# Optimization experiments

Measured on AMD Instinct MI355X. Metric: run time of the kernel, lower is better.

## Reference

```python
import jax, jax.numpy as jnp
import numpy as np

N = 100000
E = 1600000
IN_DIM, HID, OUT = 128, 64, 32
SLOPE = 0.1


def setup_inputs() -> dict:
    key = jax.random.key(0)
    ks = jax.random.split(key, 8)
    x = jax.random.normal(ks[0], (N, IN_DIM), dtype=jnp.float32)
    edge_index = jax.random.randint(ks[1], (2, E), 0, N, dtype=jnp.int64)
    s1 = 1.0 / np.sqrt(IN_DIM)
    s2 = 1.0 / np.sqrt(HID)
    W_l1 = jax.random.uniform(ks[2], (IN_DIM, HID), jnp.float32, -s1, s1)
    W_r1 = jax.random.uniform(ks[3], (IN_DIM, HID), jnp.float32, -s1, s1)
    b1 = jax.random.uniform(ks[4], (HID,), jnp.float32, -s1, s1)
    W_l2 = jax.random.uniform(ks[5], (HID, OUT), jnp.float32, -s2, s2)
    W_r2 = jax.random.uniform(ks[6], (HID, OUT), jnp.float32, -s2, s2)
    b2 = jax.random.uniform(ks[7], (OUT,), jnp.float32, -s2, s2)
    return {"x": x, "edge_index": edge_index,
            "W_l1": W_l1, "W_r1": W_r1, "b1": b1,
            "W_l2": W_l2, "W_r2": W_r2, "b2": b2}


def _sage_conv(h, src, dst, deg_inv, W_l, W_r, b):
    # mean-aggregate neighbor features: gather from src, scatter-add to dst
    agg = jax.ops.segment_sum(h[src], dst, num_segments=N) * deg_inv  # [N, d]
    return agg @ W_l + h @ W_r + b


def reference(x, edge_index, W_l1, W_r1, b1, W_l2, W_r2, b2):
    src, dst = edge_index[0], edge_index[1]
    deg = jax.ops.segment_sum(jnp.ones((E,), x.dtype), dst, num_segments=N)
    deg_inv = (1.0 / jnp.maximum(deg, 1.0))[:, None]  # [N, 1]
    h = jax.nn.leaky_relu(_sage_conv(x, src, dst, deg_inv, W_l1, W_r1, b1), SLOPE)
    z = jax.nn.leaky_relu(_sage_conv(h, src, dst, deg_inv, W_l2, W_r2, b2), SLOPE)
    return z
```

## Files before the change

### kernel.cpp

```cpp
#include <hip/hip_runtime.h>


constexpr int IN_DIM  = 128;
constexpr int HID     = 64;
constexpr int OUT_DIM = 32;
constexpr float SLOPE = 0.1f;
constexpr int NPB_SHIFT = 8;
constexpr int NBMAX = 512;
constexpr int CHUNK = 4096;
constexpr int SUBCAP = 4096;

typedef unsigned int uint32;
typedef unsigned short ushort16;

__device__ inline float blo(uint32 u) { return __uint_as_float(u << 16); }
__device__ inline float bhi(uint32 u) { return __uint_as_float(u & 0xffff0000u); }
__device__ inline ushort16 f2b(float f) {
    uint32 u = __float_as_uint(f);
    u += 0x7fffu + ((u >> 16) & 1u);
    return (ushort16)(u >> 16);
}
__device__ inline uint32 pack2(float lo, float hi) {
    return (uint32)f2b(lo) | ((uint32)f2b(hi) << 16);
}
__device__ inline float lrelu(float v) { return (v > 0.f) ? v : SLOPE * v; }
__device__ inline void addup(float* acc, uint4 u) {
    acc[0] += blo(u.x); acc[1] += bhi(u.x);
    acc[2] += blo(u.y); acc[3] += bhi(u.y);
    acc[4] += blo(u.z); acc[5] += bhi(u.z);
    acc[6] += blo(u.w); acc[7] += bhi(u.w);
}

__global__ __launch_bounds__(256) void prep_kernel(
    const float* __restrict__ Wl1, const float* __restrict__ Wr1,
    const float* __restrict__ Wl2, const float* __restrict__ Wr2,
    ushort16* __restrict__ Wb1, ushort16* __restrict__ Wb2,
    int* __restrict__ bhist, int* __restrict__ done) {
    const int gid = blockIdx.x * 256 + threadIdx.x;
    if (gid < NBMAX) bhist[gid] = 0;
    if (gid == NBMAX) *done = 0;
    for (int i = gid; i < 128 * 128; i += gridDim.x * 256) {
        int c = i >> 7, k = i & 127;
        Wb1[i] = f2b((c < HID) ? Wl1[k * HID + c] : Wr1[k * HID + (c - HID)]);
    }
    for (int i = gid; i < 64 * 64; i += gridDim.x * 256) {
        int c = i >> 6, k = i & 63;
        Wb2[i] = f2b((c < OUT_DIM) ? Wl2[k * OUT_DIM + c]
                                   : Wr2[k * OUT_DIM + (c - OUT_DIM)]);
    }
}

__global__ __launch_bounds__(256) void hist_scan_kernel(
    const int* __restrict__ dst, int* __restrict__ bhist,
    int* __restrict__ pbase, int* __restrict__ bcur,
    int* __restrict__ done, int E, int NB) {
    __shared__ int bh[NBMAX];
    __shared__ int s2[256];
    __shared__ int flag;
    const int tid = threadIdx.x;
    for (int i = tid; i < NBMAX; i += 256) bh[i] = 0;
    __syncthreads();
    for (int e = blockIdx.x * 256 + tid; e < E; e += gridDim.x * 256)
        atomicAdd(&bh[dst[e] >> NPB_SHIFT], 1);
    __syncthreads();
    for (int b = tid; b < NBMAX; b += 256)
        if (bh[b]) atomicAdd(&bhist[b], bh[b]);
    __threadfence();
    if (tid == 0) flag = (atomicAdd(done, 1) == (int)gridDim.x - 1) ? 1 : 0;
    __syncthreads();
    if (!flag) return;
    __threadfence();
    int v0 = atomicAdd(&bhist[2 * tid], 0);
    int v1 = atomicAdd(&bhist[2 * tid + 1], 0);
    int p0 = (v0 + 15) & ~15, p1 = (v1 + 15) & ~15;
    s2[tid] = p0 + p1; __syncthreads();
    for (int off = 1; off < 256; off <<= 1) {
        int b = (tid >= off) ? s2[tid - off] : 0;
        __syncthreads();
        s2[tid] += b;
        __syncthreads();
    }
    int base = s2[tid] - (p0 + p1);
    pbase[2 * tid]     = base;      bcur[2 * tid]     = base;
    pbase[2 * tid + 1] = base + p0; bcur[2 * tid + 1] = base + p0;
}

__global__ __launch_bounds__(256) void gemm1_part_kernel(
    const float* __restrict__ x, const ushort16* __restrict__ Wb1,
    const float* __restrict__ b1,
    const int* __restrict__ src, const int* __restrict__ dst,
    int* __restrict__ bcur, uint32* __restrict__ pairs,
    ushort16* __restrict__ xl, float* __restrict__ xr,
    int N, int E, int NB, int npart) {
    using frag = __attribute__((ext_vector_type(8))) short;
    using f32x4 = __attribute__((ext_vector_type(4))) float;
    constexpr int LDA = IN_DIM + 8;
    __shared__ union {
        struct {
            int hist[NBMAX], loff[NBMAX], cur[NBMAX], gbase[NBMAX];
            int s[256];
            uint32 stage[CHUNK];
        } p;
        ushort16 Ash[64][LDA];
    } sm;
    const int tid = threadIdx.x;
    if (blockIdx.x < npart) {
        const int e0  = blockIdx.x * CHUNK;
        const int cnt = min(CHUNK, E - e0);
        for (int i = tid; i < NBMAX; i += 256) sm.p.hist[i] = 0;
        __syncthreads();
        int sreg[16], dreg[16];
#pragma unroll
        for (int k = 0; k < 16; ++k) {
            int i = tid + k * 256;
            if (i < cnt) {
                sreg[k] = src[e0 + i];
                dreg[k] = dst[e0 + i];
                atomicAdd(&sm.p.hist[dreg[k] >> NPB_SHIFT], 1);
            }
        }
        __syncthreads();
        int a0 = sm.p.hist[2 * tid], a1 = sm.p.hist[2 * tid + 1];
        sm.p.s[tid] = a0 + a1; __syncthreads();
        for (int off = 1; off < 256; off <<= 1) {
            int t = (tid >= off) ? sm.p.s[tid - off] : 0;
            __syncthreads();
            sm.p.s[tid] += t;
            __syncthreads();
        }
        int ex = sm.p.s[tid] - (a0 + a1);
        sm.p.loff[2 * tid] = ex;      sm.p.loff[2 * tid + 1] = ex + a0;
        sm.p.cur[2 * tid]  = ex;      sm.p.cur[2 * tid + 1]  = ex + a0;
        __syncthreads();
#pragma unroll
        for (int k = 0; k < 16; ++k) {
            int i = tid + k * 256;
            if (i < cnt) {
                int b = dreg[k] >> NPB_SHIFT;
                int pos = atomicAdd(&sm.p.cur[b], 1);
                sm.p.stage[pos] = (uint32)sreg[k] | ((uint32)(dreg[k] & 255) << 24);
            }
        }
        __syncthreads();
        for (int b = tid; b < NB; b += 256) {
            int cb = sm.p.hist[b];
            if (cb) sm.p.gbase[b] = atomicAdd(&bcur[b], cb);
        }
        __syncthreads();
        for (int i = tid; i < cnt; i += 256) {
            int lo = 0, hi = NB - 1;
            while (lo < hi) {
                int mid = (lo + hi + 1) >> 1;
                if (sm.p.loff[mid] <= i) lo = mid; else hi = mid - 1;
            }
            pairs[sm.p.gbase[lo] + (i - sm.p.loff[lo])] = sm.p.stage[i];
        }
        return;
    }
    const int n0 = (blockIdx.x - npart) * 64;
    {
        const int lc = (tid & 31) * 4;
        for (int row = tid >> 5; row < 64; row += 8) {
            int node = n0 + row;
            float4 xv = (node < N)
                ? *reinterpret_cast<const float4*>(&x[(long)node * IN_DIM + lc])
                : float4{0.f, 0.f, 0.f, 0.f};
            ushort16 pk[4] = {f2b(xv.x), f2b(xv.y), f2b(xv.z), f2b(xv.w)};
            *reinterpret_cast<ushort2*>(&sm.Ash[row][lc])     = ushort2{pk[0], pk[1]};
            *reinterpret_cast<ushort2*>(&sm.Ash[row][lc + 2]) = ushort2{pk[2], pk[3]};
        }
    }
    __syncthreads();
    const int lane = tid & 63;
    const int m0   = (tid >> 6) * 16;
    const int mlo  = lane & 15;
    const int qk   = lane >> 4;
    frag Af[4];
#pragma unroll
    for (int kc = 0; kc < 4; ++kc)
        Af[kc] = *reinterpret_cast<const frag*>(&sm.Ash[m0 + mlo][kc * 32 + qk * 8]);
#pragma unroll
    for (int ct = 0; ct < 8; ++ct) {
        f32x4 acc = {0.f, 0.f, 0.f, 0.f};
#pragma unroll
        for (int kc = 0; kc < 4; ++kc) {
            frag Bf = *reinterpret_cast<const frag*>(
                &Wb1[(ct * 16 + mlo) * 128 + kc * 32 + qk * 8]);
            acc = __builtin_amdgcn_mfma_f32_16x16x32_bf16(Af[kc], Bf, acc, 0, 0, 0);
        }
        const int col = ct * 16 + mlo;
#pragma unroll
        for (int r = 0; r < 4; ++r) {
            int node = n0 + m0 + qk * 4 + r;
            if (node < N) {
                if (col < HID) xl[(long)node * HID + col] = f2b(acc[r]);
                else           xr[(long)node * HID + (col - HID)] = acc[r] + b1[col - HID];
            }
        }
    }
}

__global__ __launch_bounds__(512) void agg1_gemm2_kernel(
    const uint32* __restrict__ pairs, const int* __restrict__ bhist,
    const int* __restrict__ pbase,
    const uint4* __restrict__ xlq, const float* __restrict__ xr,
    const ushort16* __restrict__ Wb2, const float* __restrict__ b2,
    uint32* __restrict__ srcs, int* __restrict__ rowptr, int* __restrict__ degA,
    ushort16* __restrict__ hl, float* __restrict__ hr, int N) {
    using frag = __attribute__((ext_vector_type(8))) short;
    using f32x4 = __attribute__((ext_vector_type(4))) float;
    constexpr int LDH = HID + 8;
    __shared__ int hist[256], loff[256], cur[128];
    __shared__ int lsrc[SUBCAP];
    __shared__ ushort16 hsh[128][LDH];
    const int tid  = threadIdx.x;
    const int bkt  = blockIdx.x >> 1;
    const int half = blockIdx.x & 1;
    const int n0   = bkt << NPB_SHIFT;
    const int base = pbase[bkt];
    const int sz   = bhist[bkt];
    if (tid < 256) hist[tid] = 0;
    __syncthreads();
    for (int i = tid; i < sz; i += 512)
        atomicAdd(&hist[pairs[base + i] >> 24], 1);
    __syncthreads();
    int v = (tid < 256) ? hist[tid] : 0;
    if (tid < 256) loff[tid] = v;
    __syncthreads();
    for (int off = 1; off < 256; off <<= 1) {
        int t = (tid >= off && tid < 256) ? loff[tid - off] : 0;
        __syncthreads();
        if (tid < 256) loff[tid] += t;
        __syncthreads();
    }
    if (tid < 256) loff[tid] -= v;
    __syncthreads();
    if (half == 0 && tid < 256 && n0 + tid < N) {
        rowptr[n0 + tid] = base + loff[tid];
        degA[n0 + tid]   = hist[tid];
    }
    const int hbase = loff[half << 7];
    const int hcnt  = (half ? sz : loff[128]) - hbase;
    if (tid < 128) cur[tid] = loff[(half << 7) + tid] - hbase;
    __syncthreads();
    for (int i = tid; i < sz; i += 512) {
        uint32 u = pairs[base + i];
        int dl = u >> 24;
        if ((dl >> 7) == half) {
            int pos = atomicAdd(&cur[dl & 127], 1);
            lsrc[pos] = (int)(u & 0xFFFFFFu);
        }
    }
    __syncthreads();
    for (int i = tid; i < hcnt; i += 512)
        srcs[base + hbase + i] = (uint32)lsrc[i];
    const int lane = tid & 63;
    const int wid  = tid >> 6;
    const int li   = lane & 7;
    const int eh   = (lane >> 3) & 1;
    const int nw   = lane >> 4;
    for (int pass = 0; pass < 4; ++pass) {
        const int nll = pass * 32 + wid * 4 + nw;
        const int nl  = (half << 7) + nll;
        const int n   = n0 + nl;
        if (n < N) {
            const int lo0 = loff[nl] - hbase;
            const int d   = hist[nl];
            const int jb  = eh ? (d >> 1) : 0;
            const int je  = eh ? d : (d >> 1);
            float acc[8] = {};
            if (jb < je) {
                int j = jb;
                do {
                    int i0[8];
#pragma unroll
                    for (int t = 0; t < 8; ++t) {
                        int jj = j + t;
                        i0[t] = lsrc[lo0 + (jj < je ? jj : je - 1)];
                    }
                    uint4 u0[8];
#pragma unroll
                    for (int t = 0; t < 8; ++t) u0[t] = xlq[(long)i0[t] * 8 + li];
#pragma unroll
                    for (int t = 0; t < 8; ++t)
                        if (j + t < je) addup(acc, u0[t]);
                    j += 8;
                } while (j < je);
            }
#pragma unroll
            for (int t = 0; t < 8; ++t) acc[t] += __shfl_xor(acc[t], 8);
            if (eh == 0) {
                const float dinv = (d > 0) ? (1.f / (float)d) : 1.f;
                float4 xrA = *reinterpret_cast<const float4*>(&xr[(long)n * HID + 8 * li]);
                float4 xrB = *reinterpret_cast<const float4*>(&xr[(long)n * HID + 8 * li + 4]);
                float h[8];
                h[0] = fmaf(acc[0], dinv, xrA.x); h[1] = fmaf(acc[1], dinv, xrA.y);
                h[2] = fmaf(acc[2], dinv, xrA.z); h[3] = fmaf(acc[3], dinv, xrA.w);
                h[4] = fmaf(acc[4], dinv, xrB.x); h[5] = fmaf(acc[5], dinv, xrB.y);
                h[6] = fmaf(acc[6], dinv, xrB.z); h[7] = fmaf(acc[7], dinv, xrB.w);
#pragma unroll
                for (int t = 0; t < 8; ++t) h[t] = lrelu(h[t]);
                uint4 pk;
                pk.x = pack2(h[0], h[1]); pk.y = pack2(h[2], h[3]);
                pk.z = pack2(h[4], h[5]); pk.w = pack2(h[6], h[7]);
                *reinterpret_cast<uint4*>(&hsh[nll][li * 8]) = pk;
            }
        }
    }
    __syncthreads();
    const int m0  = wid * 16;
    const int mlo = lane & 15;
    const int qk  = lane >> 4;
    frag Af[2];
#pragma unroll
    for (int kc = 0; kc < 2; ++kc)
        Af[kc] = *reinterpret_cast<const frag*>(&hsh[m0 + mlo][kc * 32 + qk * 8]);
#pragma unroll
    for (int ct = 0; ct < 4; ++ct) {
        f32x4 acc = {0.f, 0.f, 0.f, 0.f};
#pragma unroll
        for (int kc = 0; kc < 2; ++kc) {
            frag Bf = *reinterpret_cast<const frag*>(
                &Wb2[(ct * 16 + mlo) * 64 + kc * 32 + qk * 8]);
            acc = __builtin_amdgcn_mfma_f32_16x16x32_bf16(Af[kc], Bf, acc, 0, 0, 0);
        }
        const int col = ct * 16 + mlo;
#pragma unroll
        for (int r = 0; r < 4; ++r) {
            int node = n0 + (half << 7) + m0 + qk * 4 + r;
            if (node < N) {
                if (col < OUT_DIM) hl[(long)node * OUT_DIM + col] = f2b(acc[r]);
                else hr[(long)node * OUT_DIM + (col - OUT_DIM)] = acc[r] + b2[col - OUT_DIM];
            }
        }
    }
}

__global__ __launch_bounds__(256) void agg2_final_kernel(
    const int* __restrict__ rowptr, const int* __restrict__ degA,
    const uint32* __restrict__ srcs,
    const uint4* __restrict__ hlq, const float* __restrict__ hr,
    float* __restrict__ z, int N) {
    const int lane  = threadIdx.x & 63;
    const int li    = lane & 3;
    const int gbase = lane & 60;
    const int wave  = (blockIdx.x << 2) + (threadIdx.x >> 6);
    const int n     = wave * 16 + (lane >> 2);
    if (n >= N) return;
    const int rp = rowptr[n];
    const int d  = degA[n];
    float acc[8] = {};
    int j = 0;
    while (j + 16 <= d) {
        int sA = (int)srcs[rp + j + li];
        int sB = (int)srcs[rp + j + 4 + li];
        int sC = (int)srcs[rp + j + 8 + li];
        int sD = (int)srcs[rp + j + 12 + li];
        uint4 u[16];
#pragma unroll
        for (int t = 0; t < 4; ++t) u[t]      = hlq[(long)__shfl(sA, gbase + t) * 4 + li];
#pragma unroll
        for (int t = 0; t < 4; ++t) u[4 + t]  = hlq[(long)__shfl(sB, gbase + t) * 4 + li];
#pragma unroll
        for (int t = 0; t < 4; ++t) u[8 + t]  = hlq[(long)__shfl(sC, gbase + t) * 4 + li];
#pragma unroll
        for (int t = 0; t < 4; ++t) u[12 + t] = hlq[(long)__shfl(sD, gbase + t) * 4 + li];
#pragma unroll
        for (int t = 0; t < 16; ++t) addup(acc, u[t]);
        j += 16;
    }
    while (j + 4 <= d) {
        int sA = (int)srcs[rp + j + li];
        uint4 u[4];
#pragma unroll
        for (int t = 0; t < 4; ++t) u[t] = hlq[(long)__shfl(sA, gbase + t) * 4 + li];
#pragma unroll
        for (int t = 0; t < 4; ++t) addup(acc, u[t]);
        j += 4;
    }
    int r = d - j;
    if (r > 0) {
        int sA = (int)srcs[rp + j + ((li < r) ? li : 0)];
#pragma unroll
        for (int t = 0; t < 3; ++t) {
            if (t < r) {
                uint4 u = hlq[(long)__shfl(sA, gbase + t) * 4 + li];
                addup(acc, u);
            }
        }
    }
    const float dinv = (d > 0) ? (1.f / (float)d) : 1.f;
    float4 hA = *reinterpret_cast<const float4*>(&hr[(long)n * OUT_DIM + 8 * li]);
    float4 hB = *reinterpret_cast<const float4*>(&hr[(long)n * OUT_DIM + 8 * li + 4]);
    float4 vA, vB;
    vA.x = lrelu(fmaf(acc[0], dinv, hA.x)); vA.y = lrelu(fmaf(acc[1], dinv, hA.y));
    vA.z = lrelu(fmaf(acc[2], dinv, hA.z)); vA.w = lrelu(fmaf(acc[3], dinv, hA.w));
    vB.x = lrelu(fmaf(acc[4], dinv, hB.x)); vB.y = lrelu(fmaf(acc[5], dinv, hB.y));
    vB.z = lrelu(fmaf(acc[6], dinv, hB.z)); vB.w = lrelu(fmaf(acc[7], dinv, hB.w));
    *reinterpret_cast<float4*>(&z[(long)n * OUT_DIM + 8 * li]) = vA;
    *reinterpret_cast<float4*>(&z[(long)n * OUT_DIM + 8 * li + 4]) = vB;
}

extern "C" void kernel_launch(void* const* d_in, const int* in_sizes, int n_in,
                              void* d_out, int out_size, void* d_ws, size_t ws_size,
                              hipStream_t stream) {
    const float* x   = (const float*)d_in[0];
    const int*   ei  = (const int*)d_in[1];
    const float* Wl1 = (const float*)d_in[2];
    const float* Wr1 = (const float*)d_in[3];
    const float* b1  = (const float*)d_in[4];
    const float* Wl2 = (const float*)d_in[5];
    const float* Wr2 = (const float*)d_in[6];
    const float* b2  = (const float*)d_in[7];

    const int N = in_sizes[0] / IN_DIM;
    const int E = in_sizes[1] / 2;
    const int* src = ei;
    const int* dst = ei + E;
    const int NB = (N + 255) >> NPB_SHIFT;

    char* p = (char*)d_ws;
    int* bhist    = (int*)p;           p += sizeof(int) * NBMAX;
    int* pbase    = (int*)p;           p += sizeof(int) * NBMAX;
    int* bcur     = (int*)p;           p += sizeof(int) * NBMAX;
    int* done     = (int*)p;           p += sizeof(int) * 4;
    int* rowptr   = (int*)p;           p += sizeof(int) * (N + 4);
    int* degA     = (int*)p;           p += sizeof(int) * (N + 4);
    uint32* pairs = (uint32*)p;        p += sizeof(uint32) * ((size_t)E + 16 * NBMAX);
    uint32* srcs  = (uint32*)p;        p += sizeof(uint32) * ((size_t)E + 16 * NBMAX);
    ushort16* Wb1 = (ushort16*)p;      p += sizeof(ushort16) * 128 * 128;
    ushort16* Wb2 = (ushort16*)p;      p += sizeof(ushort16) * 64 * 64;
    ushort16* xl  = (ushort16*)p;      p += sizeof(ushort16) * (size_t)N * HID;
    float* xr     = (float*)p;         p += sizeof(float) * (size_t)N * HID;
    ushort16* hl  = (ushort16*)p;      p += sizeof(ushort16) * (size_t)N * OUT_DIM;
    float* hr     = (float*)p;         p += sizeof(float) * (size_t)N * OUT_DIM;

    const int ngemm = (N + 63) / 64;
    const int npart = (E + CHUNK - 1) / CHUNK;
    prep_kernel<<<32, 256, 0, stream>>>(Wl1, Wr1, Wl2, Wr2, Wb1, Wb2, bhist, done);
    hist_scan_kernel<<<256, 256, 0, stream>>>(dst, bhist, pbase, bcur, done, E, NB);
    gemm1_part_kernel<<<npart + ngemm, 256, 0, stream>>>(
        x, Wb1, b1, src, dst, bcur, pairs, xl, xr, N, E, NB, npart);
    agg1_gemm2_kernel<<<NB * 2, 512, 0, stream>>>(pairs, bhist, pbase,
                                                  (const uint4*)xl, xr, Wb2, b2,
                                                  srcs, rowptr, degA, hl, hr, N);
    agg2_final_kernel<<<(N + 63) / 64, 256, 0, stream>>>(rowptr, degA, srcs,
                                                         (const uint4*)hl, hr,
                                                         (float*)d_out, N);
}
```

Measured before the change: 275.0 us.

## Halve destination bucket size and restructure layer-1 aggregation to one node per lane group

Buckets shrink from 256 to 128 destination nodes, which doubles the bucket count and the number of agg1_gemm2 blocks; each block now handles 64 nodes. The scans and shared-memory arrays change to match, and gbase is folded into cur. The aggregation loop drops the split-edge shuffle reduction: each 8-lane group processes one node's full neighbor list, with 16-wide unrolled gathers plus remainder paths, and only 4 waves run the MFMA. This aims at more parallelism and less scan and shuffle overhead, at the cost of more blocks, idle waves in the GEMM phase, and a tighter SUBCAP limit on edges per half-bucket.

```diff
diff --git a/kernel.cpp b/kernel.cpp
--- a/kernel.cpp
+++ b/kernel.cpp
@@ -5,10 +5,10 @@
 constexpr int HID     = 64;
 constexpr int OUT_DIM = 32;
 constexpr float SLOPE = 0.1f;
-constexpr int NPB_SHIFT = 8;
-constexpr int NBMAX = 512;
+constexpr int NPB_SHIFT = 7;
+constexpr int NBMAX = 1024;
 constexpr int CHUNK = 4096;
-constexpr int SUBCAP = 4096;
+constexpr int SUBCAP = 2048;
 
 typedef unsigned int uint32;
 typedef unsigned short ushort16;
@@ -70,19 +70,26 @@
     __syncthreads();
     if (!flag) return;
     __threadfence();
-    int v0 = atomicAdd(&bhist[2 * tid], 0);
-    int v1 = atomicAdd(&bhist[2 * tid + 1], 0);
+    int v0 = atomicAdd(&bhist[4 * tid], 0);
+    int v1 = atomicAdd(&bhist[4 * tid + 1], 0);
+    int v2 = atomicAdd(&bhist[4 * tid + 2], 0);
+    int v3 = atomicAdd(&bhist[4 * tid + 3], 0);
     int p0 = (v0 + 15) & ~15, p1 = (v1 + 15) & ~15;
-    s2[tid] = p0 + p1; __syncthreads();
+    int p2 = (v2 + 15) & ~15, p3 = (v3 + 15) & ~15;
+    int tot = p0 + p1 + p2 + p3;
+    s2[tid] = tot; __syncthreads();
     for (int off = 1; off < 256; off <<= 1) {
         int b = (tid >= off) ? s2[tid - off] : 0;
         __syncthreads();
         s2[tid] += b;
         __syncthreads();
     }
-    int base = s2[tid] - (p0 + p1);
-    pbase[2 * tid]     = base;      bcur[2 * tid]     = base;
-    pbase[2 * tid + 1] = base + p0; bcur[2 * tid + 1] = base + p0;
+    int base = s2[tid] - tot;
+    pbase[4 * tid]     = base;           bcur[4 * tid]     = base;
+    pbase[4 * tid + 1] = base + p0;      bcur[4 * tid + 1] = base + p0;
+    pbase[4 * tid + 2] = base + p0 + p1; bcur[4 * tid + 2] = base + p0 + p1;
+    pbase[4 * tid + 3] = base + p0 + p1 + p2;
+    bcur[4 * tid + 3]  = base + p0 + p1 + p2;
 }
 
 __global__ __launch_bounds__(256) void gemm1_part_kernel(
@@ -97,7 +104,7 @@
     constexpr int LDA = IN_DIM + 8;
     __shared__ union {
         struct {
-            int hist[NBMAX], loff[NBMAX], cur[NBMAX], gbase[NBMAX];
+            int hist[NBMAX], loff[NBMAX], cur[NBMAX];
             int s[256];
             uint32 stage[CHUNK];
         } p;
@@ -120,17 +127,25 @@
             }
         }
         __syncthreads();
-        int a0 = sm.p.hist[2 * tid], a1 = sm.p.hist[2 * tid + 1];
-        sm.p.s[tid] = a0 + a1; __syncthreads();
+        int a0 = sm.p.hist[4 * tid],     a1 = sm.p.hist[4 * tid + 1];
+        int a2 = sm.p.hist[4 * tid + 2], a3 = sm.p.hist[4 * tid + 3];
+        int tot = a0 + a1 + a2 + a3;
+        sm.p.s[tid] = tot; __syncthreads();
         for (int off = 1; off < 256; off <<= 1) {
             int t = (tid >= off) ? sm.p.s[tid - off] : 0;
             __syncthreads();
             sm.p.s[tid] += t;
             __syncthreads();
         }
-        int ex = sm.p.s[tid] - (a0 + a1);
-        sm.p.loff[2 * tid] = ex;      sm.p.loff[2 * tid + 1] = ex + a0;
-        sm.p.cur[2 * tid]  = ex;      sm.p.cur[2 * tid + 1]  = ex + a0;
+        int ex = sm.p.s[tid] - tot;
+        sm.p.loff[4 * tid]     = ex;
+        sm.p.loff[4 * tid + 1] = ex + a0;
+        sm.p.loff[4 * tid + 2] = ex + a0 + a1;
+        sm.p.loff[4 * tid + 3] = ex + a0 + a1 + a2;
+        sm.p.cur[4 * tid]      = ex;
+        sm.p.cur[4 * tid + 1]  = ex + a0;
+        sm.p.cur[4 * tid + 2]  = ex + a0 + a1;
+        sm.p.cur[4 * tid + 3]  = ex + a0 + a1 + a2;
         __syncthreads();
 #pragma unroll
         for (int k = 0; k < 16; ++k) {
@@ -138,13 +153,13 @@
             if (i < cnt) {
                 int b = dreg[k] >> NPB_SHIFT;
                 int pos = atomicAdd(&sm.p.cur[b], 1);
-                sm.p.stage[pos] = (uint32)sreg[k] | ((uint32)(dreg[k] & 255) << 24);
+                sm.p.stage[pos] = (uint32)sreg[k] | ((uint32)(dreg[k] & 127) << 24);
             }
         }
         __syncthreads();
         for (int b = tid; b < NB; b += 256) {
             int cb = sm.p.hist[b];
-            if (cb) sm.p.gbase[b] = atomicAdd(&bcur[b], cb);
+            if (cb) sm.p.cur[b] = atomicAdd(&bcur[b], cb);
         }
         __syncthreads();
         for (int i = tid; i < cnt; i += 256) {
@@ -153,7 +168,7 @@
                 int mid = (lo + hi + 1) >> 1;
                 if (sm.p.loff[mid] <= i) lo = mid; else hi = mid - 1;
             }
-            pairs[sm.p.gbase[lo] + (i - sm.p.loff[lo])] = sm.p.stage[i];
+            pairs[sm.p.cur[lo] + (i - sm.p.loff[lo])] = sm.p.stage[i];
         }
         return;
     }
@@ -210,44 +225,44 @@
     using frag = __attribute__((ext_vector_type(8))) short;
     using f32x4 = __attribute__((ext_vector_type(4))) float;
     constexpr int LDH = HID + 8;
-    __shared__ int hist[256], loff[256], cur[128];
+    __shared__ int hist[128], loff[128], cur[64];
     __shared__ int lsrc[SUBCAP];
-    __shared__ ushort16 hsh[128][LDH];
+    __shared__ ushort16 hsh[64][LDH];
     const int tid  = threadIdx.x;
     const int bkt  = blockIdx.x >> 1;
     const int half = blockIdx.x & 1;
     const int n0   = bkt << NPB_SHIFT;
     const int base = pbase[bkt];
     const int sz   = bhist[bkt];
-    if (tid < 256) hist[tid] = 0;
+    if (tid < 128) hist[tid] = 0;
     __syncthreads();
     for (int i = tid; i < sz; i += 512)
         atomicAdd(&hist[pairs[base + i] >> 24], 1);
     __syncthreads();
-    int v = (tid < 256) ? hist[tid] : 0;
-    if (tid < 256) loff[tid] = v;
-    __syncthreads();
-    for (int off = 1; off < 256; off <<= 1) {
-        int t = (tid >= off && tid < 256) ? loff[tid - off] : 0;
-        __syncthreads();
-        if (tid < 256) loff[tid] += t;
-        __syncthreads();
-    }
-    if (tid < 256) loff[tid] -= v;
-    __syncthreads();
-    if (half == 0 && tid < 256 && n0 + tid < N) {
+    int v = (tid < 128) ? hist[tid] : 0;
+    if (tid < 128) loff[tid] = v;
+    __syncthreads();
+    for (int off = 1; off < 128; off <<= 1) {
+        int t = (tid >= off && tid < 128) ? loff[tid - off] : 0;
+        __syncthreads();
+        if (tid < 128) loff[tid] += t;
+        __syncthreads();
+    }
+    if (tid < 128) loff[tid] -= v;
+    __syncthreads();
+    if (half == 0 && tid < 128 && n0 + tid < N) {
         rowptr[n0 + tid] = base + loff[tid];
         degA[n0 + tid]   = hist[tid];
     }
-    const int hbase = loff[half << 7];
-    const int hcnt  = (half ? sz : loff[128]) - hbase;
-    if (tid < 128) cur[tid] = loff[(half << 7) + tid] - hbase;
+    const int hbase = loff[half << 6];
+    const int hcnt  = (half ? sz : loff[64]) - hbase;
+    if (tid < 64) cur[tid] = loff[(half << 6) + tid] - hbase;
     __syncthreads();
     for (int i = tid; i < sz; i += 512) {
         uint32 u = pairs[base + i];
         int dl = u >> 24;
-        if ((dl >> 7) == half) {
-            int pos = atomicAdd(&cur[dl & 127], 1);
+        if ((dl >> 6) == half) {
+            int pos = atomicAdd(&cur[dl & 63], 1);
             lsrc[pos] = (int)(u & 0xFFFFFFu);
         }
     }
@@ -257,80 +272,86 @@
     const int lane = tid & 63;
     const int wid  = tid >> 6;
     const int li   = lane & 7;
-    const int eh   = (lane >> 3) & 1;
-    const int nw   = lane >> 4;
-    for (int pass = 0; pass < 4; ++pass) {
-        const int nll = pass * 32 + wid * 4 + nw;
-        const int nl  = (half << 7) + nll;
-        const int n   = n0 + nl;
+    {
+        const int nlb = wid * 8 + (lane >> 3);
+        const int n   = n0 + (half << 6) + nlb;
         if (n < N) {
-            const int lo0 = loff[nl] - hbase;
-            const int d   = hist[nl];
-            const int jb  = eh ? (d >> 1) : 0;
-            const int je  = eh ? d : (d >> 1);
+            const int lo0 = loff[(half << 6) + nlb] - hbase;
+            const int d   = hist[(half << 6) + nlb];
             float acc[8] = {};
-            if (jb < je) {
-                int j = jb;
-                do {
-                    int i0[8];
-#pragma unroll
-                    for (int t = 0; t < 8; ++t) {
-                        int jj = j + t;
-                        i0[t] = lsrc[lo0 + (jj < je ? jj : je - 1)];
-                    }
-                    uint4 u0[8];
-#pragma unroll
-                    for (int t = 0; t < 8; ++t) u0[t] = xlq[(long)i0[t] * 8 + li];
-#pragma unroll
-                    for (int t = 0; t < 8; ++t)
-                        if (j + t < je) addup(acc, u0[t]);
-                    j += 8;
-                } while (j < je);
-            }
-#pragma unroll
-            for (int t = 0; t < 8; ++t) acc[t] += __shfl_xor(acc[t], 8);
-            if (eh == 0) {
-                const float dinv = (d > 0) ? (1.f / (float)d) : 1.f;
-                float4 xrA = *reinterpret_cast<const float4*>(&xr[(long)n * HID + 8 * li]);
-                float4 xrB = *reinterpret_cast<const float4*>(&xr[(long)n * HID + 8 * li + 4]);
-                float h[8];
-                h[0] = fmaf(acc[0], dinv, xrA.x); h[1] = fmaf(acc[1], dinv, xrA.y);
-                h[2] = fmaf(acc[2], dinv, xrA.z); h[3] = fmaf(acc[3], dinv, xrA.w);
-                h[4] = fmaf(acc[4], dinv, xrB.x); h[5] = fmaf(acc[5], dinv, xrB.y);
-                h[6] = fmaf(acc[6], dinv, xrB.z); h[7] = fmaf(acc[7], dinv, xrB.w);
-#pragma unroll
-                for (int t = 0; t < 8; ++t) h[t] = lrelu(h[t]);
-                uint4 pk;
-                pk.x = pack2(h[0], h[1]); pk.y = pack2(h[2], h[3]);
-                pk.z = pack2(h[4], h[5]); pk.w = pack2(h[6], h[7]);
-                *reinterpret_cast<uint4*>(&hsh[nll][li * 8]) = pk;
-            }
-        }
-    }
-    __syncthreads();
-    const int m0  = wid * 16;
-    const int mlo = lane & 15;
-    const int qk  = lane >> 4;
-    frag Af[2];
-#pragma unroll
-    for (int kc = 0; kc < 2; ++kc)
-        Af[kc] = *reinterpret_cast<const frag*>(&hsh[m0 + mlo][kc * 32 + qk * 8]);
-#pragma unroll
-    for (int ct = 0; ct < 4; ++ct) {
-        f32x4 acc = {0.f, 0.f, 0.f, 0.f};
-#pragma unroll
-        for (int kc = 0; kc < 2; ++kc) {
-            frag Bf = *reinterpret_cast<const frag*>(
-                &Wb2[(ct * 16 + mlo) * 64 + kc * 32 + qk * 8]);
-            acc = __builtin_amdgcn_mfma_f32_16x16x32_bf16(Af[kc], Bf, acc, 0, 0, 0);
-        }
-        const int col = ct * 16 + mlo;
-#pragma unroll
-        for (int r = 0; r < 4; ++r) {
-            int node = n0 + (half << 7) + m0 + qk * 4 + r;
-            if (node < N) {
-                if (col < OUT_DIM) hl[(long)node * OUT_DIM + col] = f2b(acc[r]);
-                else hr[(long)node * OUT_DIM + (col - OUT_DIM)] = acc[r] + b2[col - OUT_DIM];
+            int j = 0;
+            while (j + 16 <= d) {
+                int i0[8], i1[8];
+#pragma unroll
+                for (int t = 0; t < 8; ++t) i0[t] = lsrc[lo0 + j + t];
+#pragma unroll
+                for (int t = 0; t < 8; ++t) i1[t] = lsrc[lo0 + j + 8 + t];
+                uint4 u0[8], u1[8];
+#pragma unroll
+                for (int t = 0; t < 8; ++t) u0[t] = xlq[(long)i0[t] * 8 + li];
+#pragma unroll
+                for (int t = 0; t < 8; ++t) u1[t] = xlq[(long)i1[t] * 8 + li];
+#pragma unroll
+                for (int t = 0; t < 8; ++t) { addup(acc, u0[t]); addup(acc, u1[t]); }
+                j += 16;
+            }
+            if (j + 8 <= d) {
+                int i0[8];
+#pragma unroll
+                for (int t = 0; t < 8; ++t) i0[t] = lsrc[lo0 + j + t];
+                uint4 u0[8];
+#pragma unroll
+                for (int t = 0; t < 8; ++t) u0[t] = xlq[(long)i0[t] * 8 + li];
+#pragma unroll
+                for (int t = 0; t < 8; ++t) addup(acc, u0[t]);
+                j += 8;
+            }
+            for (; j < d; ++j) {
+                uint4 u = xlq[(long)lsrc[lo0 + j] * 8 + li];
+                addup(acc, u);
+            }
+            const float dinv = (d > 0) ? (1.f / (float)d) : 1.f;
+            float4 xrA = *reinterpret_cast<const float4*>(&xr[(long)n * HID + 8 * li]);
+            float4 xrB = *reinterpret_cast<const float4*>(&xr[(long)n * HID + 8 * li + 4]);
+            float h[8];
+            h[0] = fmaf(acc[0], dinv, xrA.x); h[1] = fmaf(acc[1], dinv, xrA.y);
+            h[2] = fmaf(acc[2], dinv, xrA.z); h[3] = fmaf(acc[3], dinv, xrA.w);
+            h[4] = fmaf(acc[4], dinv, xrB.x); h[5] = fmaf(acc[5], dinv, xrB.y);
+            h[6] = fmaf(acc[6], dinv, xrB.z); h[7] = fmaf(acc[7], dinv, xrB.w);
+#pragma unroll
+            for (int t = 0; t < 8; ++t) h[t] = lrelu(h[t]);
+            uint4 pk;
+            pk.x = pack2(h[0], h[1]); pk.y = pack2(h[2], h[3]);
+            pk.z = pack2(h[4], h[5]); pk.w = pack2(h[6], h[7]);
+            *reinterpret_cast<uint4*>(&hsh[nlb][li * 8]) = pk;
+        }
+    }
+    __syncthreads();
+    if (wid < 4) {
+        const int m0  = wid * 16;
+        const int mlo = lane & 15;
+        const int qk  = lane >> 4;
+        frag Af[2];
+#pragma unroll
+        for (int kc = 0; kc < 2; ++kc)
+            Af[kc] = *reinterpret_cast<const frag*>(&hsh[m0 + mlo][kc * 32 + qk * 8]);
+#pragma unroll
+        for (int ct = 0; ct < 4; ++ct) {
+            f32x4 acc = {0.f, 0.f, 0.f, 0.f};
+#pragma unroll
+            for (int kc = 0; kc < 2; ++kc) {
+                frag Bf = *reinterpret_cast<const frag*>(
+                    &Wb2[(ct * 16 + mlo) * 64 + kc * 32 + qk * 8]);
+                acc = __builtin_amdgcn_mfma_f32_16x16x32_bf16(Af[kc], Bf, acc, 0, 0, 0);
+            }
+            const int col = ct * 16 + mlo;
+#pragma unroll
+            for (int r = 0; r < 4; ++r) {
+                int node = n0 + (half << 6) + m0 + qk * 4 + r;
+                if (node < N) {
+                    if (col < OUT_DIM) hl[(long)node * OUT_DIM + col] = f2b(acc[r]);
+                    else hr[(long)node * OUT_DIM + (col - OUT_DIM)] = acc[r] + b2[col - OUT_DIM];
+                }
             }
         }
     }
@@ -417,13 +438,13 @@
     const int E = in_sizes[1] / 2;
     const int* src = ei;
     const int* dst = ei + E;
-    const int NB = (N + 255) >> NPB_SHIFT;
+    const int NB = (N + 127) >> NPB_SHIFT;
 
     char* p = (char*)d_ws;
     int* bhist    = (int*)p;           p += sizeof(int) * NBMAX;
+    int* done     = (int*)p;           p += sizeof(int) * 4;
     int* pbase    = (int*)p;           p += sizeof(int) * NBMAX;
     int* bcur     = (int*)p;           p += sizeof(int) * NBMAX;
-    int* done     = (int*)p;           p += sizeof(int) * 4;
     int* rowptr   = (int*)p;           p += sizeof(int) * (N + 4);
     int* degA     = (int*)p;           p += sizeof(int) * (N + 4);
     uint32* pairs = (uint32*)p;        p += sizeof(uint32) * ((size_t)E + 16 * NBMAX);
```

New measurement: 285.7 us. +3.9%, slower.

## Store layer-1 neighbor features as FP8 and regather with 4 lanes per node

Applied to the files above, without the earlier changes.

The layer-1 projected neighbor features (xl) are now stored as FP8 instead of BF16, which halves the bytes moved in the random gather of the first aggregation. The aggregation loop is restructured so each node uses 4 lanes of 16 features each, with one lane group covering all of its edges. The old split of edges across two half-warps and the shuffle reduction are removed. This lowers gather traffic but adds precision loss from FP8 quantization, which could break tolerance, and spreads work unevenly across lanes for nodes with different degrees.

```diff
diff --git a/kernel.cpp b/kernel.cpp
--- a/kernel.cpp
+++ b/kernel.cpp
@@ -12,6 +12,8 @@
 
 typedef unsigned int uint32;
 typedef unsigned short ushort16;
+typedef unsigned char uchar8;
+using floatx2 = __attribute__((ext_vector_type(2))) float;
 
 __device__ inline float blo(uint32 u) { return __uint_as_float(u << 16); }
 __device__ inline float bhi(uint32 u) { return __uint_as_float(u & 0xffff0000u); }
@@ -29,6 +31,19 @@
     acc[2] += blo(u.y); acc[3] += bhi(u.y);
     acc[4] += blo(u.z); acc[5] += bhi(u.z);
     acc[6] += blo(u.w); acc[7] += bhi(u.w);
+}
+__device__ inline uchar8 f2fp8(float f) {
+    uint32 r = (uint32)__builtin_amdgcn_cvt_pk_fp8_f32(f, f, 0, false);
+    return (uchar8)(r & 0xffu);
+}
+__device__ inline void addp4(float* acc, uint32 w) {
+    floatx2 a = __builtin_amdgcn_cvt_pk_f32_fp8((int)w, false);
+    floatx2 b = __builtin_amdgcn_cvt_pk_f32_fp8((int)w, true);
+    acc[0] += a[0]; acc[1] += a[1]; acc[2] += b[0]; acc[3] += b[1];
+}
+__device__ inline void addq(float* acc, uint4 u) {
+    addp4(acc + 0, u.x); addp4(acc + 4, u.y);
+    addp4(acc + 8, u.z); addp4(acc + 12, u.w);
 }
 
 __global__ __launch_bounds__(256) void prep_kernel(
@@ -90,7 +105,7 @@
     const float* __restrict__ b1,
     const int* __restrict__ src, const int* __restrict__ dst,
     int* __restrict__ bcur, uint32* __restrict__ pairs,
-    ushort16* __restrict__ xl, float* __restrict__ xr,
+    uchar8* __restrict__ xlb, float* __restrict__ xr,
     int N, int E, int NB, int npart) {
     using frag = __attribute__((ext_vector_type(8))) short;
     using f32x4 = __attribute__((ext_vector_type(4))) float;
@@ -193,7 +208,7 @@
         for (int r = 0; r < 4; ++r) {
             int node = n0 + m0 + qk * 4 + r;
             if (node < N) {
-                if (col < HID) xl[(long)node * HID + col] = f2b(acc[r]);
+                if (col < HID) xlb[(long)node * HID + col] = f2fp8(acc[r]);
                 else           xr[(long)node * HID + (col - HID)] = acc[r] + b1[col - HID];
             }
         }
@@ -256,55 +271,70 @@
         srcs[base + hbase + i] = (uint32)lsrc[i];
     const int lane = tid & 63;
     const int wid  = tid >> 6;
-    const int li   = lane & 7;
-    const int eh   = (lane >> 3) & 1;
-    const int nw   = lane >> 4;
-    for (int pass = 0; pass < 4; ++pass) {
-        const int nll = pass * 32 + wid * 4 + nw;
-        const int nl  = (half << 7) + nll;
+    const int li   = lane & 3;
+    {
+        const int nlb = wid * 16 + (lane >> 2);
+        const int nl  = (half << 7) + nlb;
         const int n   = n0 + nl;
         if (n < N) {
             const int lo0 = loff[nl] - hbase;
             const int d   = hist[nl];
-            const int jb  = eh ? (d >> 1) : 0;
-            const int je  = eh ? d : (d >> 1);
-            float acc[8] = {};
-            if (jb < je) {
-                int j = jb;
-                do {
-                    int i0[8];
-#pragma unroll
-                    for (int t = 0; t < 8; ++t) {
-                        int jj = j + t;
-                        i0[t] = lsrc[lo0 + (jj < je ? jj : je - 1)];
-                    }
-                    uint4 u0[8];
-#pragma unroll
-                    for (int t = 0; t < 8; ++t) u0[t] = xlq[(long)i0[t] * 8 + li];
-#pragma unroll
-                    for (int t = 0; t < 8; ++t)
-                        if (j + t < je) addup(acc, u0[t]);
-                    j += 8;
-                } while (j < je);
-            }
-#pragma unroll
-            for (int t = 0; t < 8; ++t) acc[t] += __shfl_xor(acc[t], 8);
-            if (eh == 0) {
-                const float dinv = (d > 0) ? (1.f / (float)d) : 1.f;
-                float4 xrA = *reinterpret_cast<const float4*>(&xr[(long)n * HID + 8 * li]);
-                float4 xrB = *reinterpret_cast<const float4*>(&xr[(long)n * HID + 8 * li + 4]);
-                float h[8];
-                h[0] = fmaf(acc[0], dinv, xrA.x); h[1] = fmaf(acc[1], dinv, xrA.y);
-                h[2] = fmaf(acc[2], dinv, xrA.z); h[3] = fmaf(acc[3], dinv, xrA.w);
-                h[4] = fmaf(acc[4], dinv, xrB.x); h[5] = fmaf(acc[5], dinv, xrB.y);
-                h[6] = fmaf(acc[6], dinv, xrB.z); h[7] = fmaf(acc[7], dinv, xrB.w);
-#pragma unroll
-                for (int t = 0; t < 8; ++t) h[t] = lrelu(h[t]);
-                uint4 pk;
-                pk.x = pack2(h[0], h[1]); pk.y = pack2(h[2], h[3]);
-                pk.z = pack2(h[4], h[5]); pk.w = pack2(h[6], h[7]);
-                *reinterpret_cast<uint4*>(&hsh[nll][li * 8]) = pk;
-            }
+            float acc[16] = {};
+            int j = 0;
+            while (j + 16 <= d) {
+                int i0[8], i1[8];
+#pragma unroll
+                for (int t = 0; t < 8; ++t) i0[t] = lsrc[lo0 + j + t];
+#pragma unroll
+                for (int t = 0; t < 8; ++t) i1[t] = lsrc[lo0 + j + 8 + t];
+                uint4 u0[8], u1[8];
+#pragma unroll
+                for (int t = 0; t < 8; ++t) u0[t] = xlq[(long)i0[t] * 4 + li];
+#pragma unroll
+                for (int t = 0; t < 8; ++t) u1[t] = xlq[(long)i1[t] * 4 + li];
+#pragma unroll
+                for (int t = 0; t < 8; ++t) { addq(acc, u0[t]); addq(acc, u1[t]); }
+                j += 16;
+            }
+            if (j + 8 <= d) {
+                int i0[8];
+#pragma unroll
+                for (int t = 0; t < 8; ++t) i0[t] = lsrc[lo0 + j + t];
+                uint4 u0[8];
+#pragma unroll
+                for (int t = 0; t < 8; ++t) u0[t] = xlq[(long)i0[t] * 4 + li];
+#pragma unroll
+                for (int t = 0; t < 8; ++t) addq(acc, u0[t]);
+                j += 8;
+            }
+            for (; j < d; ++j) {
+                uint4 u = xlq[(long)lsrc[lo0 + j] * 4 + li];
+                addq(acc, u);
+            }
+            const float dinv = (d > 0) ? (1.f / (float)d) : 1.f;
+            const float* xrp = &xr[(long)n * HID + li * 16];
+            float4 xa = *reinterpret_cast<const float4*>(xrp);
+            float4 xb = *reinterpret_cast<const float4*>(xrp + 4);
+            float4 xc = *reinterpret_cast<const float4*>(xrp + 8);
+            float4 xd = *reinterpret_cast<const float4*>(xrp + 12);
+            float hv[16];
+            hv[0]  = fmaf(acc[0],  dinv, xa.x); hv[1]  = fmaf(acc[1],  dinv, xa.y);
+            hv[2]  = fmaf(acc[2],  dinv, xa.z); hv[3]  = fmaf(acc[3],  dinv, xa.w);
+            hv[4]  = fmaf(acc[4],  dinv, xb.x); hv[5]  = fmaf(acc[5],  dinv, xb.y);
+            hv[6]  = fmaf(acc[6],  dinv, xb.z); hv[7]  = fmaf(acc[7],  dinv, xb.w);
+            hv[8]  = fmaf(acc[8],  dinv, xc.x); hv[9]  = fmaf(acc[9],  dinv, xc.y);
+            hv[10] = fmaf(acc[10], dinv, xc.z); hv[11] = fmaf(acc[11], dinv, xc.w);
+            hv[12] = fmaf(acc[12], dinv, xd.x); hv[13] = fmaf(acc[13], dinv, xd.y);
+            hv[14] = fmaf(acc[14], dinv, xd.z); hv[15] = fmaf(acc[15], dinv, xd.w);
+#pragma unroll
+            for (int t = 0; t < 16; ++t) hv[t] = lrelu(hv[t]);
+            uint4 pk0, pk1;
+            pk0.x = pack2(hv[0],  hv[1]);  pk0.y = pack2(hv[2],  hv[3]);
+            pk0.z = pack2(hv[4],  hv[5]);  pk0.w = pack2(hv[6],  hv[7]);
+            pk1.x = pack2(hv[8],  hv[9]);  pk1.y = pack2(hv[10], hv[11]);
+            pk1.z = pack2(hv[12], hv[13]); pk1.w = pack2(hv[14], hv[15]);
+            *reinterpret_cast<uint4*>(&hsh[nlb][li * 16])     = pk0;
+            *reinterpret_cast<uint4*>(&hsh[nlb][li * 16 + 8]) = pk1;
         }
     }
     __syncthreads();
@@ -421,16 +451,16 @@
 
     char* p = (char*)d_ws;
     int* bhist    = (int*)p;           p += sizeof(int) * NBMAX;
+    int* done     = (int*)p;           p += sizeof(int) * 4;
     int* pbase    = (int*)p;           p += sizeof(int) * NBMAX;
     int* bcur     = (int*)p;           p += sizeof(int) * NBMAX;
-    int* done     = (int*)p;           p += sizeof(int) * 4;
     int* rowptr   = (int*)p;           p += sizeof(int) * (N + 4);
     int* degA     = (int*)p;           p += sizeof(int) * (N + 4);
     uint32* pairs = (uint32*)p;        p += sizeof(uint32) * ((size_t)E + 16 * NBMAX);
     uint32* srcs  = (uint32*)p;        p += sizeof(uint32) * ((size_t)E + 16 * NBMAX);
     ushort16* Wb1 = (ushort16*)p;      p += sizeof(ushort16) * 128 * 128;
     ushort16* Wb2 = (ushort16*)p;      p += sizeof(ushort16) * 64 * 64;
-    ushort16* xl  = (ushort16*)p;      p += sizeof(ushort16) * (size_t)N * HID;
+    uchar8* xlb   = (uchar8*)p;        p += sizeof(uchar8) * ((size_t)N * HID + 64);
     float* xr     = (float*)p;         p += sizeof(float) * (size_t)N * HID;
     ushort16* hl  = (ushort16*)p;      p += sizeof(ushort16) * (size_t)N * OUT_DIM;
     float* hr     = (float*)p;         p += sizeof(float) * (size_t)N * OUT_DIM;
@@ -440,9 +470,9 @@
     prep_kernel<<<32, 256, 0, stream>>>(Wl1, Wr1, Wl2, Wr2, Wb1, Wb2, bhist, done);
     hist_scan_kernel<<<256, 256, 0, stream>>>(dst, bhist, pbase, bcur, done, E, NB);
     gemm1_part_kernel<<<npart + ngemm, 256, 0, stream>>>(
-        x, Wb1, b1, src, dst, bcur, pairs, xl, xr, N, E, NB, npart);
+        x, Wb1, b1, src, dst, bcur, pairs, xlb, xr, N, E, NB, npart);
     agg1_gemm2_kernel<<<NB * 2, 512, 0, stream>>>(pairs, bhist, pbase,
-                                                  (const uint4*)xl, xr, Wb2, b2,
+                                                  (const uint4*)xlb, xr, Wb2, b2,
                                                   srcs, rowptr, degA, hl, hr, N);
     agg2_final_kernel<<<(N + 63) / 64, 256, 0, stream>>>(rowptr, degA, srcs,
                                                          (const uint4*)hl, hr,
```

Result: slower. 284.4 us (+3.4%).

## Store layer-2 neighbor features in FP8 and restructure layer-1 aggregation loop

Applied to the files above, without the earlier changes.

The second-layer neighbor projection hl is now stored as FP8 (one byte per element) instead of bf16, halving the gather traffic in the final aggregation kernel, which decodes with packed fp8-to-f32 conversions. The layer-1 aggregation drops the split of each node's edges across two half-wave groups. Each 8-lane group now handles a whole node, over 2 passes instead of 4, with 16-wide unrolled gathers and a scalar tail. FP8 storage adds quantization error to the aggregated features, and the per-node loop may lose load balance on high-degree nodes.

```diff
diff --git a/kernel.cpp b/kernel.cpp
--- a/kernel.cpp
+++ b/kernel.cpp
@@ -12,6 +12,8 @@
 
 typedef unsigned int uint32;
 typedef unsigned short ushort16;
+typedef unsigned char uchar8;
+using floatx2 = __attribute__((ext_vector_type(2))) float;
 
 __device__ inline float blo(uint32 u) { return __uint_as_float(u << 16); }
 __device__ inline float bhi(uint32 u) { return __uint_as_float(u & 0xffff0000u); }
@@ -29,6 +31,18 @@
     acc[2] += blo(u.y); acc[3] += bhi(u.y);
     acc[4] += blo(u.z); acc[5] += bhi(u.z);
     acc[6] += blo(u.w); acc[7] += bhi(u.w);
+}
+__device__ inline uchar8 f2fp8(float f) {
+    uint32 r = (uint32)__builtin_amdgcn_cvt_pk_fp8_f32(f, f, 0, false);
+    return (uchar8)(r & 0xffu);
+}
+__device__ inline void addp4(float* acc, uint32 w) {
+    floatx2 a = __builtin_amdgcn_cvt_pk_f32_fp8((int)w, false);
+    floatx2 b = __builtin_amdgcn_cvt_pk_f32_fp8((int)w, true);
+    acc[0] += a[0]; acc[1] += a[1]; acc[2] += b[0]; acc[3] += b[1];
+}
+__device__ inline void addq8(float* acc, uint2 u) {
+    addp4(acc + 0, u.x); addp4(acc + 4, u.y);
 }
 
 __global__ __launch_bounds__(256) void prep_kernel(
@@ -206,7 +220,7 @@
     const uint4* __restrict__ xlq, const float* __restrict__ xr,
     const ushort16* __restrict__ Wb2, const float* __restrict__ b2,
     uint32* __restrict__ srcs, int* __restrict__ rowptr, int* __restrict__ degA,
-    ushort16* __restrict__ hl, float* __restrict__ hr, int N) {
+    uchar8* __restrict__ hl8, float* __restrict__ hr, int N) {
     using frag = __attribute__((ext_vector_type(8))) short;
     using f32x4 = __attribute__((ext_vector_type(4))) float;
     constexpr int LDH = HID + 8;
@@ -257,55 +271,60 @@
     const int lane = tid & 63;
     const int wid  = tid >> 6;
     const int li   = lane & 7;
-    const int eh   = (lane >> 3) & 1;
-    const int nw   = lane >> 4;
-    for (int pass = 0; pass < 4; ++pass) {
-        const int nll = pass * 32 + wid * 4 + nw;
+#pragma unroll
+    for (int pass = 0; pass < 2; ++pass) {
+        const int nll = pass * 64 + wid * 8 + (lane >> 3);
         const int nl  = (half << 7) + nll;
         const int n   = n0 + nl;
-        if (n < N) {
-            const int lo0 = loff[nl] - hbase;
-            const int d   = hist[nl];
-            const int jb  = eh ? (d >> 1) : 0;
-            const int je  = eh ? d : (d >> 1);
-            float acc[8] = {};
-            if (jb < je) {
-                int j = jb;
-                do {
-                    int i0[8];
-#pragma unroll
-                    for (int t = 0; t < 8; ++t) {
-                        int jj = j + t;
-                        i0[t] = lsrc[lo0 + (jj < je ? jj : je - 1)];
-                    }
-                    uint4 u0[8];
-#pragma unroll
-                    for (int t = 0; t < 8; ++t) u0[t] = xlq[(long)i0[t] * 8 + li];
-#pragma unroll
-                    for (int t = 0; t < 8; ++t)
-                        if (j + t < je) addup(acc, u0[t]);
-                    j += 8;
-                } while (j < je);
-            }
-#pragma unroll
-            for (int t = 0; t < 8; ++t) acc[t] += __shfl_xor(acc[t], 8);
-            if (eh == 0) {
-                const float dinv = (d > 0) ? (1.f / (float)d) : 1.f;
-                float4 xrA = *reinterpret_cast<const float4*>(&xr[(long)n * HID + 8 * li]);
-                float4 xrB = *reinterpret_cast<const float4*>(&xr[(long)n * HID + 8 * li + 4]);
-                float h[8];
-                h[0] = fmaf(acc[0], dinv, xrA.x); h[1] = fmaf(acc[1], dinv, xrA.y);
-                h[2] = fmaf(acc[2], dinv, xrA.z); h[3] = fmaf(acc[3], dinv, xrA.w);
-                h[4] = fmaf(acc[4], dinv, xrB.x); h[5] = fmaf(acc[5], dinv, xrB.y);
-                h[6] = fmaf(acc[6], dinv, xrB.z); h[7] = fmaf(acc[7], dinv, xrB.w);
-#pragma unroll
-                for (int t = 0; t < 8; ++t) h[t] = lrelu(h[t]);
-                uint4 pk;
-                pk.x = pack2(h[0], h[1]); pk.y = pack2(h[2], h[3]);
-                pk.z = pack2(h[4], h[5]); pk.w = pack2(h[6], h[7]);
-                *reinterpret_cast<uint4*>(&hsh[nll][li * 8]) = pk;
-            }
-        }
+        if (n >= N) continue;
+        const int lo0 = loff[nl] - hbase;
+        const int d   = hist[nl];
+        float acc[8] = {};
+        int j = 0;
+        while (j + 16 <= d) {
+            int i0[8], i1[8];
+#pragma unroll
+            for (int t = 0; t < 8; ++t) i0[t] = lsrc[lo0 + j + t];
+#pragma unroll
+            for (int t = 0; t < 8; ++t) i1[t] = lsrc[lo0 + j + 8 + t];
+            uint4 u0[8], u1[8];
+#pragma unroll
+            for (int t = 0; t < 8; ++t) u0[t] = xlq[(long)i0[t] * 8 + li];
+#pragma unroll
+            for (int t = 0; t < 8; ++t) u1[t] = xlq[(long)i1[t] * 8 + li];
+#pragma unroll
+            for (int t = 0; t < 8; ++t) { addup(acc, u0[t]); addup(acc, u1[t]); }
+            j += 16;
+        }
+        if (j + 8 <= d) {
+            int i0[8];
+#pragma unroll
+            for (int t = 0; t < 8; ++t) i0[t] = lsrc[lo0 + j + t];
+            uint4 u0[8];
+#pragma unroll
+            for (int t = 0; t < 8; ++t) u0[t] = xlq[(long)i0[t] * 8 + li];
+#pragma unroll
+            for (int t = 0; t < 8; ++t) addup(acc, u0[t]);
+            j += 8;
+        }
+        for (; j < d; ++j) {
+            uint4 u = xlq[(long)lsrc[lo0 + j] * 8 + li];
+            addup(acc, u);
+        }
+        const float dinv = (d > 0) ? (1.f / (float)d) : 1.f;
+        float4 xrA = *reinterpret_cast<const float4*>(&xr[(long)n * HID + 8 * li]);
+        float4 xrB = *reinterpret_cast<const float4*>(&xr[(long)n * HID + 8 * li + 4]);
+        float h[8];
+        h[0] = fmaf(acc[0], dinv, xrA.x); h[1] = fmaf(acc[1], dinv, xrA.y);
+        h[2] = fmaf(acc[2], dinv, xrA.z); h[3] = fmaf(acc[3], dinv, xrA.w);
+        h[4] = fmaf(acc[4], dinv, xrB.x); h[5] = fmaf(acc[5], dinv, xrB.y);
+        h[6] = fmaf(acc[6], dinv, xrB.z); h[7] = fmaf(acc[7], dinv, xrB.w);
+#pragma unroll
+        for (int t = 0; t < 8; ++t) h[t] = lrelu(h[t]);
+        uint4 pk;
+        pk.x = pack2(h[0], h[1]); pk.y = pack2(h[2], h[3]);
+        pk.z = pack2(h[4], h[5]); pk.w = pack2(h[6], h[7]);
+        *reinterpret_cast<uint4*>(&hsh[nll][li * 8]) = pk;
     }
     __syncthreads();
     const int m0  = wid * 16;
@@ -329,7 +348,7 @@
         for (int r = 0; r < 4; ++r) {
             int node = n0 + (half << 7) + m0 + qk * 4 + r;
             if (node < N) {
-                if (col < OUT_DIM) hl[(long)node * OUT_DIM + col] = f2b(acc[r]);
+                if (col < OUT_DIM) hl8[(long)node * OUT_DIM + col] = f2fp8(acc[r]);
                 else hr[(long)node * OUT_DIM + (col - OUT_DIM)] = acc[r] + b2[col - OUT_DIM];
             }
         }
@@ -339,7 +358,7 @@
 __global__ __launch_bounds__(256) void agg2_final_kernel(
     const int* __restrict__ rowptr, const int* __restrict__ degA,
     const uint32* __restrict__ srcs,
-    const uint4* __restrict__ hlq, const float* __restrict__ hr,
+    const uint2* __restrict__ hlq, const float* __restrict__ hr,
     float* __restrict__ z, int N) {
     const int lane  = threadIdx.x & 63;
     const int li    = lane & 3;
@@ -356,7 +375,7 @@
         int sB = (int)srcs[rp + j + 4 + li];
         int sC = (int)srcs[rp + j + 8 + li];
         int sD = (int)srcs[rp + j + 12 + li];
-        uint4 u[16];
+        uint2 u[16];
 #pragma unroll
         for (int t = 0; t < 4; ++t) u[t]      = hlq[(long)__shfl(sA, gbase + t) * 4 + li];
 #pragma unroll
@@ -366,16 +385,16 @@
 #pragma unroll
         for (int t = 0; t < 4; ++t) u[12 + t] = hlq[(long)__shfl(sD, gbase + t) * 4 + li];
 #pragma unroll
-        for (int t = 0; t < 16; ++t) addup(acc, u[t]);
+        for (int t = 0; t < 16; ++t) addq8(acc, u[t]);
         j += 16;
     }
     while (j + 4 <= d) {
         int sA = (int)srcs[rp + j + li];
-        uint4 u[4];
+        uint2 u[4];
 #pragma unroll
         for (int t = 0; t < 4; ++t) u[t] = hlq[(long)__shfl(sA, gbase + t) * 4 + li];
 #pragma unroll
-        for (int t = 0; t < 4; ++t) addup(acc, u[t]);
+        for (int t = 0; t < 4; ++t) addq8(acc, u[t]);
         j += 4;
     }
     int r = d - j;
@@ -384,8 +403,8 @@
 #pragma unroll
         for (int t = 0; t < 3; ++t) {
             if (t < r) {
-                uint4 u = hlq[(long)__shfl(sA, gbase + t) * 4 + li];
-                addup(acc, u);
+                uint2 u = hlq[(long)__shfl(sA, gbase + t) * 4 + li];
+                addq8(acc, u);
             }
         }
     }
@@ -421,9 +440,9 @@
 
     char* p = (char*)d_ws;
     int* bhist    = (int*)p;           p += sizeof(int) * NBMAX;
+    int* done     = (int*)p;           p += sizeof(int) * 4;
     int* pbase    = (int*)p;           p += sizeof(int) * NBMAX;
     int* bcur     = (int*)p;           p += sizeof(int) * NBMAX;
-    int* done     = (int*)p;           p += sizeof(int) * 4;
     int* rowptr   = (int*)p;           p += sizeof(int) * (N + 4);
     int* degA     = (int*)p;           p += sizeof(int) * (N + 4);
     uint32* pairs = (uint32*)p;        p += sizeof(uint32) * ((size_t)E + 16 * NBMAX);
@@ -432,7 +451,7 @@
     ushort16* Wb2 = (ushort16*)p;      p += sizeof(ushort16) * 64 * 64;
     ushort16* xl  = (ushort16*)p;      p += sizeof(ushort16) * (size_t)N * HID;
     float* xr     = (float*)p;         p += sizeof(float) * (size_t)N * HID;
-    ushort16* hl  = (ushort16*)p;      p += sizeof(ushort16) * (size_t)N * OUT_DIM;
+    uchar8* hl8   = (uchar8*)p;        p += sizeof(uchar8) * ((size_t)N * OUT_DIM + 64);
     float* hr     = (float*)p;         p += sizeof(float) * (size_t)N * OUT_DIM;
 
     const int ngemm = (N + 63) / 64;
@@ -443,8 +462,8 @@
         x, Wb1, b1, src, dst, bcur, pairs, xl, xr, N, E, NB, npart);
     agg1_gemm2_kernel<<<NB * 2, 512, 0, stream>>>(pairs, bhist, pbase,
                                                   (const uint4*)xl, xr, Wb2, b2,
-                                                  srcs, rowptr, degA, hl, hr, N);
+                                                  srcs, rowptr, degA, hl8, hr, N);
     agg2_final_kernel<<<(N + 63) / 64, 256, 0, stream>>>(rowptr, degA, srcs,
-                                                         (const uint4*)hl, hr,
+                                                         (const uint2*)hl8, hr,
                                                          (float*)d_out, N);
 }
```

Result: no change. 278.7 us (+1.4%).
